# Kernel tuning notes

Hardware: AMD Instinct MI355X
Metric: run time of the kernel (lower is better)

The kernel has to match this reference:

```python
import jax, jax.numpy as jnp
import numpy as np

IN_DIM = 512
OUT_DIM = 512
B = 2
N = 50000


def setup_inputs() -> dict:
    key = jax.random.key(0)
    k_z, k_s, k_m = jax.random.split(key, 3)
    z = jax.random.normal(k_z, (B, N, IN_DIM), dtype=jnp.float32)
    s = jax.random.normal(k_s, (B, OUT_DIM), dtype=jnp.float32)
    # torch_geometric uniform(in_dim, mat): U(-1/sqrt(in_dim), 1/sqrt(in_dim))
    bound = 1.0 / np.sqrt(IN_DIM)
    mat = jax.random.uniform(k_m, (IN_DIM, OUT_DIM), dtype=jnp.float32,
                             minval=-bound, maxval=bound)
    return {"z": z, "s": s, "mat": mat}


def reference(z, s, mat):
    # (z @ mat * s[:, None, :]).sum(dim=2).sigmoid()
    # z: [B, N, in_dim], mat: [in_dim, out_dim], s: [B, out_dim] -> [B, N]
    scores = jnp.einsum('bnd,de,be->bn', z, mat, s)
    return jax.nn.sigmoid(scores)
```

## Files before the change

### kernel.cpp

```cpp
#include <hip/hip_runtime.h>
#include <math.h>

#define IN_DIM  512
#define OUT_DIM 512
#define BATCH   2
#define NPTS    50000
#define TOTAL   (BATCH * NPTS)

__global__ __launch_bounds__(256) void dgi_compute_v(
    const float* __restrict__ mat, const float* __restrict__ s,
    float* __restrict__ v)
{
    const int b     = blockIdx.x >> 3;
    const int chunk = blockIdx.x & 7;

    __shared__ float4 s_sh[OUT_DIM / 4];
    if (threadIdx.x < OUT_DIM / 4) {
        s_sh[threadIdx.x] =
            reinterpret_cast<const float4*>(s + (size_t)b * OUT_DIM)[threadIdx.x];
    }
    __syncthreads();

    const int wave = threadIdx.x >> 6;
    const int lane = threadIdx.x & 63;

    #pragma unroll 4
    for (int i = 0; i < 16; ++i) {
        const int d = chunk * 64 + i * 4 + wave;
        const float4* mrow =
            reinterpret_cast<const float4*>(mat + (size_t)d * OUT_DIM);
        const float4 m0 = mrow[lane];
        const float4 m1 = mrow[lane + 64];
        const float4 s0 = s_sh[lane];
        const float4 s1 = s_sh[lane + 64];
        float acc = m0.x * s0.x + m0.y * s0.y + m0.z * s0.z + m0.w * s0.w
                  + m1.x * s1.x + m1.y * s1.y + m1.z * s1.z + m1.w * s1.w;
        #pragma unroll
        for (int off = 32; off; off >>= 1) acc += __shfl_xor(acc, off);
        if (lane == 0) v[b * IN_DIM + d] = acc;
    }
}

__global__ __launch_bounds__(256) void dgi_score(
    const float* __restrict__ z, const float* __restrict__ v,
    float* __restrict__ out)
{
    const int lane   = threadIdx.x & 63;
    const int wave   = (blockIdx.x * blockDim.x + threadIdx.x) >> 6;
    const int nwaves = (gridDim.x * blockDim.x) >> 6;

    int   b_cur = -1;
    float4 v0, v1;

    for (int row = wave; row < TOTAL; row += nwaves) {
        const int b = (row >= NPTS) ? 1 : 0;
        if (b != b_cur) {
            b_cur = b;
            const float4* vr =
                reinterpret_cast<const float4*>(v + (size_t)b * IN_DIM);
            v0 = vr[lane];
            v1 = vr[lane + 64];
        }
        const float4* zr =
            reinterpret_cast<const float4*>(z + (size_t)row * IN_DIM);
        const float4 z0 = zr[lane];
        const float4 z1 = zr[lane + 64];

        float acc = z0.x * v0.x + z0.y * v0.y + z0.z * v0.z + z0.w * v0.w
                  + z1.x * v1.x + z1.y * v1.y + z1.z * v1.z + z1.w * v1.w;

        #pragma unroll
        for (int off = 32; off; off >>= 1) acc += __shfl_xor(acc, off);

        if (lane == 0) {
            out[row] = 1.0f / (1.0f + __expf(-acc));
        }
    }
}

extern "C" void kernel_launch(void* const* d_in, const int* in_sizes, int n_in,
                              void* d_out, int out_size, void* d_ws, size_t ws_size,
                              hipStream_t stream) {
    const float* z   = (const float*)d_in[0];
    const float* s   = (const float*)d_in[1];
    const float* mat = (const float*)d_in[2];
    float* out = (float*)d_out;
    float* v   = (float*)d_ws;

    dgi_compute_v<<<BATCH * 8, 256, 0, stream>>>(mat, s, v);
    dgi_score<<<2048, 256, 0, stream>>>(z, v, out);
}
```

Before: 44.59 us.

## Widen v-precompute grid, use contiguous row chunks with paired nontemporal z loads

The v = mat·s precompute now assigns one wave per output element across 256 blocks instead of 16 blocks looping, which shortens the serial prologue. The scoring kernel replaces the grid-stride loop with contiguous 14-row chunks per wave. Each wave processes two rows per iteration with nontemporal loads to keep more memory requests in flight on the 400MB z stream. The launch grid grows to about 1786 blocks, sized exactly to the row count.

```diff
diff --git a/kernel.cpp b/kernel.cpp
--- a/kernel.cpp
+++ b/kernel.cpp
@@ -6,75 +6,99 @@
 #define BATCH   2
 #define NPTS    50000
 #define TOTAL   (BATCH * NPTS)
+#define RPW     14
+
+typedef float f4 __attribute__((ext_vector_type(4)));
+
+__device__ __forceinline__ f4 ntload(const f4* p) {
+    return __builtin_nontemporal_load(p);
+}
+
+__device__ __forceinline__ float dot8(f4 a0, f4 a1, f4 b0, f4 b1) {
+    return a0[0]*b0[0] + a0[1]*b0[1] + a0[2]*b0[2] + a0[3]*b0[3]
+         + a1[0]*b1[0] + a1[1]*b1[1] + a1[2]*b1[2] + a1[3]*b1[3];
+}
+
+__device__ __forceinline__ float wred(float x) {
+    #pragma unroll
+    for (int off = 32; off; off >>= 1) x += __shfl_xor(x, off);
+    return x;
+}
 
 __global__ __launch_bounds__(256) void dgi_compute_v(
     const float* __restrict__ mat, const float* __restrict__ s,
     float* __restrict__ v)
 {
-    const int b     = blockIdx.x >> 3;
-    const int chunk = blockIdx.x & 7;
+    const int lane = threadIdx.x & 63;
+    const int W    = (int)((blockIdx.x * blockDim.x + threadIdx.x) >> 6);
+    const int b    = W >> 9;
+    const int d    = W & 511;
 
-    __shared__ float4 s_sh[OUT_DIM / 4];
-    if (threadIdx.x < OUT_DIM / 4) {
-        s_sh[threadIdx.x] =
-            reinterpret_cast<const float4*>(s + (size_t)b * OUT_DIM)[threadIdx.x];
-    }
-    __syncthreads();
+    const f4* mrow = reinterpret_cast<const f4*>(mat + (size_t)d * OUT_DIM);
+    const f4* srow = reinterpret_cast<const f4*>(s   + (size_t)b * OUT_DIM);
+    const f4 m0 = mrow[lane], m1 = mrow[lane + 64];
+    const f4 s0 = srow[lane], s1 = srow[lane + 64];
 
-    const int wave = threadIdx.x >> 6;
-    const int lane = threadIdx.x & 63;
-
-    #pragma unroll 4
-    for (int i = 0; i < 16; ++i) {
-        const int d = chunk * 64 + i * 4 + wave;
-        const float4* mrow =
-            reinterpret_cast<const float4*>(mat + (size_t)d * OUT_DIM);
-        const float4 m0 = mrow[lane];
-        const float4 m1 = mrow[lane + 64];
-        const float4 s0 = s_sh[lane];
-        const float4 s1 = s_sh[lane + 64];
-        float acc = m0.x * s0.x + m0.y * s0.y + m0.z * s0.z + m0.w * s0.w
-                  + m1.x * s1.x + m1.y * s1.y + m1.z * s1.z + m1.w * s1.w;
-        #pragma unroll
-        for (int off = 32; off; off >>= 1) acc += __shfl_xor(acc, off);
-        if (lane == 0) v[b * IN_DIM + d] = acc;
-    }
+    float acc = wred(dot8(m0, m1, s0, s1));
+    if (lane == 0) v[b * IN_DIM + d] = acc;
 }
 
 __global__ __launch_bounds__(256) void dgi_score(
     const float* __restrict__ z, const float* __restrict__ v,
     float* __restrict__ out)
 {
-    const int lane   = threadIdx.x & 63;
-    const int wave   = (blockIdx.x * blockDim.x + threadIdx.x) >> 6;
-    const int nwaves = (gridDim.x * blockDim.x) >> 6;
+    const int lane = threadIdx.x & 63;
+    const int wave = (int)((blockIdx.x * blockDim.x + threadIdx.x) >> 6);
+    const long base = (long)wave * RPW;
+    if (base >= TOTAL) return;
+    const int cnt = (TOTAL - base < RPW) ? (int)(TOTAL - base) : RPW;
 
-    int   b_cur = -1;
-    float4 v0, v1;
+    int b_cur = -1;
+    f4 v0, v1;
 
-    for (int row = wave; row < TOTAL; row += nwaves) {
-        const int b = (row >= NPTS) ? 1 : 0;
+    int i = 0;
+    for (; i + 1 < cnt; i += 2) {
+        const long rowA = base + i;
+        const long rowB = rowA + 1;
+        const f4* zA = reinterpret_cast<const f4*>(z + rowA * IN_DIM);
+        const f4* zB = reinterpret_cast<const f4*>(z + rowB * IN_DIM);
+        const f4 a0 = ntload(zA + lane), a1 = ntload(zA + lane + 64);
+        const f4 c0 = ntload(zB + lane), c1 = ntload(zB + lane + 64);
+
+        const int bA = (rowA >= NPTS);
+        if (bA != b_cur) {
+            b_cur = bA;
+            const f4* vr = reinterpret_cast<const f4*>(v + (size_t)bA * IN_DIM);
+            v0 = vr[lane]; v1 = vr[lane + 64];
+        }
+        float accA = dot8(a0, a1, v0, v1);
+
+        const int bB = (rowB >= NPTS);
+        if (bB != b_cur) {
+            b_cur = bB;
+            const f4* vr = reinterpret_cast<const f4*>(v + (size_t)bB * IN_DIM);
+            v0 = vr[lane]; v1 = vr[lane + 64];
+        }
+        float accB = dot8(c0, c1, v0, v1);
+
+        accA = wred(accA);
+        accB = wred(accB);
+        if (lane == 0) {
+            out[rowA] = 1.0f / (1.0f + __expf(-accA));
+            out[rowB] = 1.0f / (1.0f + __expf(-accB));
+        }
+    }
+    if (i < cnt) {
+        const long row = base + i;
+        const f4* zr = reinterpret_cast<const f4*>(z + row * IN_DIM);
+        const f4 a0 = ntload(zr + lane), a1 = ntload(zr + lane + 64);
+        const int b = (row >= NPTS);
         if (b != b_cur) {
-            b_cur = b;
-            const float4* vr =
-                reinterpret_cast<const float4*>(v + (size_t)b * IN_DIM);
-            v0 = vr[lane];
-            v1 = vr[lane + 64];
+            const f4* vr = reinterpret_cast<const f4*>(v + (size_t)b * IN_DIM);
+            v0 = vr[lane]; v1 = vr[lane + 64];
         }
-        const float4* zr =
-            reinterpret_cast<const float4*>(z + (size_t)row * IN_DIM);
-        const float4 z0 = zr[lane];
-        const float4 z1 = zr[lane + 64];
-
-        float acc = z0.x * v0.x + z0.y * v0.y + z0.z * v0.z + z0.w * v0.w
-                  + z1.x * v1.x + z1.y * v1.y + z1.z * v1.z + z1.w * v1.w;
-
-        #pragma unroll
-        for (int off = 32; off; off >>= 1) acc += __shfl_xor(acc, off);
-
-        if (lane == 0) {
-            out[row] = 1.0f / (1.0f + __expf(-acc));
-        }
+        float acc = wred(dot8(a0, a1, v0, v1));
+        if (lane == 0) out[row] = 1.0f / (1.0f + __expf(-acc));
     }
 }
 
@@ -87,6 +111,9 @@
     float* out = (float*)d_out;
     float* v   = (float*)d_ws;
 
-    dgi_compute_v<<<BATCH * 8, 256, 0, stream>>>(mat, s, v);
-    dgi_score<<<2048, 256, 0, stream>>>(z, v, out);
+    dgi_compute_v<<<BATCH * 128, 256, 0, stream>>>(mat, s, v);
+
+    const int nwaves = (TOTAL + RPW - 1) / RPW;
+    const int blocks = (nwaves + 3) / 4;
+    dgi_score<<<blocks, 256, 0, stream>>>(z, v, out);
 }
```

Result: faster. 38.69 us (-13.2%).
